# Kernel optimization log

Hardware: AMD Instinct MI355X
Metric: run time of the kernel (lower is better)

Reference implementation:

```python
import jax, jax.numpy as jnp
import numpy as np

B, H, W, C = 4, 64, 64, 128
NH, K = 4, 7
HD = C // NH
MLPD = 4 * C
EPS = 1e-5

def _ln(x, g, b):
    m = x.mean(-1, keepdims=True)
    v = ((x - m) ** 2).mean(-1, keepdims=True)
    return (x - m) * jax.lax.rsqrt(v + EPS) * g + b

def setup_inputs() -> dict:
    key = jax.random.key(0)
    ks = jax.random.split(key, 10)
    rn = lambda k, s: jax.random.normal(k, s, dtype=jnp.float32) * 0.02
    return {
        'query': jax.random.normal(ks[0], (B, H, W, C), dtype=jnp.float32),
        'key_value': jax.random.normal(ks[1], (B, H, W, C), dtype=jnp.float32),
        'g1': jnp.ones((C,), jnp.float32), 'b1': jnp.zeros((C,), jnp.float32),
        'g2': jnp.ones((C,), jnp.float32), 'b2': jnp.zeros((C,), jnp.float32),
        'g3': jnp.ones((C,), jnp.float32), 'b3': jnp.zeros((C,), jnp.float32),
        'Wq': rn(ks[2], (C, C)), 'bq': jnp.zeros((C,), jnp.float32),
        'Wkv': rn(ks[3], (C, 2 * C)), 'bkv': jnp.zeros((2 * C,), jnp.float32),
        'Wp': rn(ks[4], (C, C)), 'bp': jnp.zeros((C,), jnp.float32),
        'rpb': rn(ks[5], (NH, 2 * K - 1, 2 * K - 1)),
        'W1': rn(ks[6], (C, MLPD)), 'bm1': jnp.zeros((MLPD,), jnp.float32),
        'W2': rn(ks[7], (MLPD, C)), 'bm2': jnp.zeros((C,), jnp.float32),
    }

def _nat(qn, kvn, Wq, bq, Wkv, bkv, Wp, bp, rpb):
    # NATTEN-style 2D neighborhood attention (clamped KxK window at borders)
    q = (qn @ Wq + bq).reshape(B, H, W, NH, HD) * (HD ** -0.5)
    kv = (kvn @ Wkv + bkv).reshape(B, H, W, 2, NH, HD)
    k, v = kv[..., 0, :, :], kv[..., 1, :, :]
    ii = jnp.clip(jnp.arange(H) - K // 2, 0, H - K)[:, None] + jnp.arange(K)  # [H,K]
    jj = jnp.clip(jnp.arange(W) - K // 2, 0, W - K)[:, None] + jnp.arange(K)  # [W,K]
    def gather(t):  # [B,H,W,NH,HD] -> [B,H,W,NH,K*K,HD]
        t = jnp.take(t, ii, axis=1)   # [B,H,K,W,NH,HD]
        t = jnp.take(t, jj, axis=3)   # [B,H,K,W,K,NH,HD]
        return t.transpose(0, 1, 3, 5, 2, 4, 6).reshape(B, H, W, NH, K * K, HD)
    kn, vn = gather(k), gather(v)
    scores = jnp.einsum('bijhd,bijhnd->bijhn', q, kn)  # [B,H,W,NH,K*K]
    # relative positional bias: offsets in [-(K-1), K-1] -> index into 2K-1 table
    ri = ii - jnp.arange(H)[:, None] + (K - 1)  # [H,K]
    rj = jj - jnp.arange(W)[:, None] + (K - 1)  # [W,K]
    bias = rpb[:, ri]                   # [NH,H,K,2K-1]
    bias = jnp.take(bias, rj, axis=3)   # [NH,H,K,W,K]
    bias = bias.transpose(1, 3, 0, 2, 4).reshape(H, W, NH, K * K)
    attn = jax.nn.softmax(scores + bias[None], axis=-1)
    out = jnp.einsum('bijhn,bijhnd->bijhd', attn, vn).reshape(B, H, W, C)
    return out @ Wp + bp

def reference(query, key_value, g1, b1, g2, b2, g3, b3, Wq, bq, Wkv, bkv, Wp, bp, rpb, W1, bm1, W2, bm2):
    shortcut = key_value
    qn = _ln(query, g1, b1)
    kvn = _ln(key_value, g2, b2)
    x = shortcut + _nat(qn, kvn, Wq, bq, Wkv, bkv, Wp, bp, rpb)
    h = _ln(x, g3, b3)
    h = jax.nn.gelu(h @ W1 + bm1, approximate=False) @ W2 + bm2
    return x + h
```

## Files before the change

### kernel.cpp

```cpp
#include <hip/hip_runtime.h>
#include <math.h>

#define TOK 16384

typedef __attribute__((ext_vector_type(8))) __bf16 bf16x8;
typedef __attribute__((ext_vector_type(4))) float f32x4;

__device__ inline unsigned short f2bf(float f) {
    union { float f; unsigned int u; } v; v.f = f;
    unsigned int r = v.u + 0x7fffu + ((v.u >> 16) & 1u);
    return (unsigned short)(r >> 16);
}
__device__ inline float gelu_exact(float v) {
    return 0.5f * v * (1.0f + erff(v * 0.70710678118654752f));
}

__device__ inline void ln_body(const float* __restrict__ x, const float* __restrict__ g,
                               const float* __restrict__ b, unsigned short* __restrict__ y,
                               int tok, int lane)
{
    float2 v = ((const float2*)(x + (size_t)tok * 128))[lane];
    float s = v.x + v.y;
#pragma unroll
    for (int m = 32; m >= 1; m >>= 1) s += __shfl_xor(s, m);
    float mean = s * (1.0f / 128.0f);
    float dx = v.x - mean, dy = v.y - mean;
    float vs = dx * dx + dy * dy;
#pragma unroll
    for (int m = 32; m >= 1; m >>= 1) vs += __shfl_xor(vs, m);
    float rs = rsqrtf(vs * (1.0f / 128.0f) + 1e-5f);
    float2 gg = ((const float2*)g)[lane];
    float2 bb = ((const float2*)b)[lane];
    float ox = dx * rs * gg.x + bb.x;
    float oy = dy * rs * gg.y + bb.y;
    unsigned int pk = (unsigned int)f2bf(ox) | ((unsigned int)f2bf(oy) << 16);
    ((unsigned int*)(y + (size_t)tok * 128))[lane] = pk;
}

__global__ __launch_bounds__(256) void prep_kernel(
    const float* __restrict__ query, const float* __restrict__ key_value,
    const float* __restrict__ g1, const float* __restrict__ b1,
    const float* __restrict__ g2, const float* __restrict__ b2,
    const float* __restrict__ Wq, const float* __restrict__ Wkv,
    const float* __restrict__ Wp, const float* __restrict__ W1, const float* __restrict__ W2,
    unsigned short* __restrict__ qnh, unsigned short* __restrict__ kvnh,
    unsigned short* __restrict__ Wt)
{
    int blk = blockIdx.x, tid = threadIdx.x;
    if (blk < 8192) {
        int lane = tid & 63;
        if (blk < 4096) ln_body(query,     g1, b1, qnh,  blk * 4 + (tid >> 6), lane);
        else            ln_body(key_value, g2, b2, kvnh, (blk - 4096) * 4 + (tid >> 6), lane);
        return;
    }
    __shared__ float tile[32][33];
    int t = blk - 8192;
    const float* src; unsigned short* dst; int Kd, Nd, li;
    if      (t < 16)  { src = Wq;  dst = Wt;          Kd = 128; Nd = 128; li = t; }
    else if (t < 48)  { src = Wkv; dst = Wt + 16384;  Kd = 128; Nd = 256; li = t - 16; }
    else if (t < 64)  { src = Wp;  dst = Wt + 49152;  Kd = 128; Nd = 128; li = t - 48; }
    else if (t < 128) { src = W1;  dst = Wt + 65536;  Kd = 128; Nd = 512; li = t - 64; }
    else              { src = W2;  dst = Wt + 131072; Kd = 512; Nd = 128; li = t - 128; }
    int ntc = Nd >> 5;
    int k0 = (li / ntc) * 32, n0 = (li % ntc) * 32;
    int r = tid >> 3, c4 = (tid & 7) * 4;
    float4 v = *(const float4*)(src + (size_t)(k0 + r) * Nd + n0 + c4);
    tile[r][c4 + 0] = v.x; tile[r][c4 + 1] = v.y;
    tile[r][c4 + 2] = v.z; tile[r][c4 + 3] = v.w;
    __syncthreads();
    ushort4 o;
    o.x = f2bf(tile[c4 + 0][r]);
    o.y = f2bf(tile[c4 + 1][r]);
    o.z = f2bf(tile[c4 + 2][r]);
    o.w = f2bf(tile[c4 + 3][r]);
    *(ushort4*)(dst + (size_t)(n0 + r) * Kd + k0 + c4) = o;
}

__global__ __launch_bounds__(256) void natqkv(
    const unsigned short* __restrict__ qnh,
    const unsigned short* __restrict__ kvnh,
    const unsigned short* __restrict__ Wt,
    const float* __restrict__ bq, const float* __restrict__ bkv,
    const float* __restrict__ rpb,
    unsigned short* __restrict__ out,
    float qscale)
{
    __shared__ __align__(16) unsigned short shm[22272];
    __shared__ float rpbs[169];
    unsigned short* kS = shm;
    unsigned short* qS = shm + 8960;
    unsigned short* P  = shm;
    unsigned short* vT = shm + 14848;
    const int tid = threadIdx.x;
    const int wave = tid >> 6, lane = tid & 63;
    const int lr = lane & 15, lg = lane >> 4;
    const int bid = blockIdx.x;
    const int tile = bid & 63, h = (bid >> 6) & 3, b = bid >> 8;
    const int ti0 = (tile >> 3) * 8, tj0 = (tile & 7) * 8;
    const int hr0 = min(max(ti0 - 3, 0), 50);
    const int hc0 = min(max(tj0 - 3, 0), 50);
    const int bb = b << 12;
    if (tid < 169) rpbs[tid] = rpb[h * 169 + tid];

    const unsigned short* WtKV = Wt + 16384;

    {
        const bool vjob = wave >= 2;
        const int n0 = vjob ? 128 + h * 32 + (wave - 2) * 16 : h * 32 + wave * 16;
        const unsigned short* wrow = WtKV + (size_t)(n0 + lr) * 128;
        bf16x8 wf[4];
#pragma unroll
        for (int kk = 0; kk < 4; ++kk) wf[kk] = *(const bf16x8*)(wrow + kk * 32 + lg * 8);
#pragma unroll
        for (int rt = 0; rt < 14; ++rt) {
            int tok = bb + (hr0 + rt) * 64 + hc0 + lr;
            const unsigned short* asrc = kvnh + (size_t)tok * 128;
            f32x4 acc = {0.f, 0.f, 0.f, 0.f};
#pragma unroll
            for (int kk = 0; kk < 4; ++kk) {
                bf16x8 xf = *(const bf16x8*)(asrc + kk * 32 + lg * 8);
                acc = vjob ? __builtin_amdgcn_mfma_f32_16x16x32_bf16(xf, wf[kk], acc, 0, 0, 0)
                           : __builtin_amdgcn_mfma_f32_16x16x32_bf16(wf[kk], xf, acc, 0, 0, 0);
            }
            if (!vjob) {
                int chb = wave * 16 + lg * 4;
                float4 bs = *(const float4*)(bkv + h * 32 + chb);
                ushort4 pk;
                pk.x = f2bf(acc[0] + bs.x); pk.y = f2bf(acc[1] + bs.y);
                pk.z = f2bf(acc[2] + bs.z); pk.w = f2bf(acc[3] + bs.w);
                *(ushort4*)&kS[(rt * 16 + lr) * 40 + chb] = pk;
            } else {
                int chl = (wave - 2) * 16 + lr;
                float bs = bkv[128 + h * 32 + chl];
                ushort4 pk;
                pk.x = f2bf(acc[0] + bs); pk.y = f2bf(acc[1] + bs);
                pk.z = f2bf(acc[2] + bs); pk.w = f2bf(acc[3] + bs);
                *(ushort4*)&vT[chl * 232 + rt * 16 + lg * 4] = pk;
            }
        }
    }
    {
        const int colt = wave & 1;
        const unsigned short* wrow = Wt + (size_t)(h * 32 + colt * 16 + lr) * 128;
        bf16x8 wf[4];
#pragma unroll
        for (int kk = 0; kk < 4; ++kk) wf[kk] = *(const bf16x8*)(wrow + kk * 32 + lg * 8);
#pragma unroll
        for (int tt = 0; tt < 2; ++tt) {
            int qrt = (wave >> 1) + tt * 2;
            int qi = qrt * 16 + lr;
            int tok = bb + (ti0 + (qi >> 3)) * 64 + tj0 + (qi & 7);
            const unsigned short* asrc = qnh + (size_t)tok * 128;
            f32x4 acc = {0.f, 0.f, 0.f, 0.f};
#pragma unroll
            for (int kk = 0; kk < 4; ++kk) {
                bf16x8 xf = *(const bf16x8*)(asrc + kk * 32 + lg * 8);
                acc = __builtin_amdgcn_mfma_f32_16x16x32_bf16(wf[kk], xf, acc, 0, 0, 0);
            }
            int chb = colt * 16 + lg * 4;
            float4 bs = *(const float4*)(bq + h * 32 + chb);
            ushort4 pk;
            pk.x = f2bf((acc[0] + bs.x) * qscale); pk.y = f2bf((acc[1] + bs.y) * qscale);
            pk.z = f2bf((acc[2] + bs.z) * qscale); pk.w = f2bf((acc[3] + bs.w) * qscale);
            *(ushort4*)&qS[(qrt * 16 + lr) * 40 + chb] = pk;
        }
    }
    __syncthreads();

    bf16x8 qf = *(const bf16x8*)&qS[(wave * 16 + lr) * 40 + lg * 8];
    f32x4 S[14];
#pragma unroll
    for (int kb = 0; kb < 14; ++kb) {
        bf16x8 kf = *(const bf16x8*)&kS[(kb * 16 + lr) * 40 + lg * 8];
        f32x4 z = {0.f, 0.f, 0.f, 0.f};
        S[kb] = __builtin_amdgcn_mfma_f32_16x16x32_bf16(qf, kf, z, 0, 0, 0);
    }
    __syncthreads();

#pragma unroll
    for (int i = 0; i < 4; ++i) {
        int m = lg * 4 + i;
        int gi = ti0 + wave * 2 + (m >> 3);
        int gj = tj0 + (m & 7);
        int si = min(max(gi - 3, 0), 57), sj = min(max(gj - 3, 0), 57);
        bool cv = (unsigned)(hc0 + lr - sj) < 7u;
        int rjc = min(max(hc0 + lr - gj + 6, 0), 12);
        float mxi = -INFINITY;
#pragma unroll
        for (int kb = 0; kb < 14; ++kb) {
            bool rv = (unsigned)(hr0 + kb - si) < 7u;
            int ric = min(max(hr0 + kb - gi + 6, 0), 12);
            float bias = rpbs[rjc + ric * 13];
            float s = (rv && cv) ? S[kb][i] + bias : -1e30f;
            S[kb][i] = s;
            mxi = fmaxf(mxi, s);
        }
        mxi = fmaxf(mxi, __shfl_xor(mxi, 1));
        mxi = fmaxf(mxi, __shfl_xor(mxi, 2));
        mxi = fmaxf(mxi, __shfl_xor(mxi, 4));
        mxi = fmaxf(mxi, __shfl_xor(mxi, 8));
        float smi = 0.0f;
#pragma unroll
        for (int kb = 0; kb < 14; ++kb) {
            float e = expf(S[kb][i] - mxi);
            S[kb][i] = e;
            smi += e;
        }
        smi += __shfl_xor(smi, 1);
        smi += __shfl_xor(smi, 2);
        smi += __shfl_xor(smi, 4);
        smi += __shfl_xor(smi, 8);
        float rinv = 1.0f / smi;
#pragma unroll
        for (int kb = 0; kb < 14; ++kb)
            P[(wave * 16 + m) * 232 + kb * 16 + lr] = f2bf(S[kb][i] * rinv);
    }

    f32x4 O[2] = {};
#pragma unroll
    for (int ks = 0; ks < 7; ++ks) {
        bf16x8 pf = *(const bf16x8*)&P[(wave * 16 + lr) * 232 + ks * 32 + lg * 8];
#pragma unroll
        for (int nb = 0; nb < 2; ++nb) {
            bf16x8 vf = *(const bf16x8*)&vT[(nb * 16 + lr) * 232 + ks * 32 + lg * 8];
            O[nb] = __builtin_amdgcn_mfma_f32_16x16x32_bf16(pf, vf, O[nb], 0, 0, 0);
        }
    }
#pragma unroll
    for (int i = 0; i < 4; ++i) {
        int m = lg * 4 + i;
        int gi = ti0 + wave * 2 + (m >> 3);
        int gj = tj0 + (m & 7);
        size_t t = ((size_t)(bb + gi * 64 + gj)) * 128 + h * 32;
        out[t + lr]      = f2bf(O[0][i]);
        out[t + 16 + lr] = f2bf(O[1][i]);
    }
}

__global__ __launch_bounds__(256) void tail_kernel(
    const unsigned short* __restrict__ attnh,
    const unsigned short* __restrict__ WtP,
    const unsigned short* __restrict__ W1t,
    const unsigned short* __restrict__ W2t,
    const float* __restrict__ bp, const float* __restrict__ bm1, const float* __restrict__ bm2,
    const float* __restrict__ resk,
    const float* __restrict__ g3, const float* __restrict__ b3,
    float* __restrict__ dout)
{
    __shared__ float xs[32][132];
    __shared__ __align__(16) unsigned short xnS[32 * 136];
    __shared__ __align__(16) unsigned short hS[32 * 520];
    const int tid = threadIdx.x;
    const int wave = tid >> 6, lane = tid & 63;
    const int lr = lane & 15, lg = lane >> 4;
    const int m0 = blockIdx.x * 32;

#pragma unroll
    for (int t = 0; t < 4; ++t) {
        int j = t * 4 + wave;
        int rowt = j >> 3, colt = j & 7;
        int tok = m0 + rowt * 16 + lr;
        f32x4 acc = {0.f, 0.f, 0.f, 0.f};
#pragma unroll
        for (int kk = 0; kk < 4; ++kk) {
            bf16x8 af = *(const bf16x8*)(attnh + (size_t)tok * 128 + kk * 32 + lg * 8);
            bf16x8 wf = *(const bf16x8*)(WtP + (size_t)(colt * 16 + lr) * 128 + kk * 32 + lg * 8);
            acc = __builtin_amdgcn_mfma_f32_16x16x32_bf16(af, wf, acc, 0, 0, 0);
        }
        int gc = colt * 16 + lr;
        float bs = bp[gc];
#pragma unroll
        for (int r = 0; r < 4; ++r) {
            int row = rowt * 16 + lg * 4 + r;
            xs[row][gc] = acc[r] + bs + resk[(size_t)(m0 + row) * 128 + gc];
        }
    }
    __syncthreads();

    {
        const int r = tid >> 3, t8 = tid & 7;
        float vals[16];
#pragma unroll
        for (int jj = 0; jj < 16; ++jj) vals[jj] = xs[r][t8 * 16 + jj];
        float s = 0.0f;
#pragma unroll
        for (int jj = 0; jj < 16; ++jj) s += vals[jj];
        s += __shfl_xor(s, 1); s += __shfl_xor(s, 2); s += __shfl_xor(s, 4);
        float mean = s * (1.0f / 128.0f);
        float vv = 0.0f;
#pragma unroll
        for (int jj = 0; jj < 16; ++jj) { float d = vals[jj] - mean; vv += d * d; }
        vv += __shfl_xor(vv, 1); vv += __shfl_xor(vv, 2); vv += __shfl_xor(vv, 4);
        float rs = rsqrtf(vv * (1.0f / 128.0f) + 1e-5f);
#pragma unroll
        for (int jj = 0; jj < 4; ++jj) {
            float4 gg = ((const float4*)g3)[t8 * 4 + jj];
            float4 bb = ((const float4*)b3)[t8 * 4 + jj];
            ushort4 o;
            o.x = f2bf((vals[jj * 4 + 0] - mean) * rs * gg.x + bb.x);
            o.y = f2bf((vals[jj * 4 + 1] - mean) * rs * gg.y + bb.y);
            o.z = f2bf((vals[jj * 4 + 2] - mean) * rs * gg.z + bb.z);
            o.w = f2bf((vals[jj * 4 + 3] - mean) * rs * gg.w + bb.w);
            *(ushort4*)&xnS[r * 136 + t8 * 16 + jj * 4] = o;
        }
    }
    __syncthreads();

#pragma unroll
    for (int t = 0; t < 16; ++t) {
        int j = t * 4 + wave;
        int rowt = j >> 5, colt = j & 31;
        f32x4 acc = {0.f, 0.f, 0.f, 0.f};
#pragma unroll
        for (int kk = 0; kk < 4; ++kk) {
            bf16x8 wf = *(const bf16x8*)(W1t + (size_t)(colt * 16 + lr) * 128 + kk * 32 + lg * 8);
            bf16x8 xf = *(const bf16x8*)&xnS[(rowt * 16 + lr) * 136 + kk * 32 + lg * 8];
            acc = __builtin_amdgcn_mfma_f32_16x16x32_bf16(wf, xf, acc, 0, 0, 0);
        }
        int chb = colt * 16 + lg * 4;
        float4 bs = *(const float4*)(bm1 + chb);
        ushort4 pk;
        pk.x = f2bf(gelu_exact(acc[0] + bs.x));
        pk.y = f2bf(gelu_exact(acc[1] + bs.y));
        pk.z = f2bf(gelu_exact(acc[2] + bs.z));
        pk.w = f2bf(gelu_exact(acc[3] + bs.w));
        *(ushort4*)&hS[(rowt * 16 + lr) * 520 + chb] = pk;
    }
    __syncthreads();

#pragma unroll
    for (int t = 0; t < 4; ++t) {
        int j = t * 4 + wave;
        int rowt = j >> 3, colt = j & 7;
        f32x4 acc = {0.f, 0.f, 0.f, 0.f};
#pragma unroll
        for (int kk = 0; kk < 16; ++kk) {
            bf16x8 hf = *(const bf16x8*)&hS[(rowt * 16 + lr) * 520 + kk * 32 + lg * 8];
            bf16x8 wf = *(const bf16x8*)(W2t + (size_t)(colt * 16 + lr) * 512 + kk * 32 + lg * 8);
            acc = __builtin_amdgcn_mfma_f32_16x16x32_bf16(hf, wf, acc, 0, 0, 0);
        }
        int gc = colt * 16 + lr;
        float bs = bm2[gc];
#pragma unroll
        for (int r = 0; r < 4; ++r) {
            int row = rowt * 16 + lg * 4 + r;
            dout[(size_t)(m0 + row) * 128 + gc] = acc[r] + bs + xs[row][gc];
        }
    }
}

extern "C" void kernel_launch(void* const* d_in, const int* in_sizes, int n_in,
                              void* d_out, int out_size, void* d_ws, size_t ws_size,
                              hipStream_t stream) {
    const float* query     = (const float*)d_in[0];
    const float* key_value = (const float*)d_in[1];
    const float* g1 = (const float*)d_in[2];
    const float* b1 = (const float*)d_in[3];
    const float* g2 = (const float*)d_in[4];
    const float* b2 = (const float*)d_in[5];
    const float* g3 = (const float*)d_in[6];
    const float* b3 = (const float*)d_in[7];
    const float* Wq  = (const float*)d_in[8];
    const float* bq  = (const float*)d_in[9];
    const float* Wkv = (const float*)d_in[10];
    const float* bkv = (const float*)d_in[11];
    const float* Wp  = (const float*)d_in[12];
    const float* bp  = (const float*)d_in[13];
    const float* rpb = (const float*)d_in[14];
    const float* W1  = (const float*)d_in[15];
    const float* bm1 = (const float*)d_in[16];
    const float* W2  = (const float*)d_in[17];
    const float* bm2 = (const float*)d_in[18];

    char* ws = (char*)d_ws;
    unsigned short* qnh   = (unsigned short*)(ws + 0);
    unsigned short* kvnh  = (unsigned short*)(ws + 4194304);
    unsigned short* attnh = (unsigned short*)(ws + 8388608);
    unsigned short* Wt    = (unsigned short*)(ws + 12582912);

    const float qscale = 0.17677669529663687f;

    prep_kernel<<<8384, 256, 0, stream>>>(query, key_value, g1, b1, g2, b2,
                                          Wq, Wkv, Wp, W1, W2, qnh, kvnh, Wt);
    natqkv<<<1024, 256, 0, stream>>>(qnh, kvnh, Wt, bq, bkv, rpb, attnh, qscale);
    tail_kernel<<<512, 256, 0, stream>>>(attnh, Wt + 49152, Wt + 65536, Wt + 131072,
                                         bp, bm1, bm2, key_value, g3, b3, (float*)d_out);
}
```

Before: 198.8 us.

## Split QKV projection from attention, fuse LayerNorm into projection kernel

Moves the LayerNorm of query and key_value into a new per-token kernel that also does the Q/K/V projections. This removes the redundant halo K/V recomputation the attention kernel did for every 8x8 tile. The attention kernel now only gathers precomputed bf16 K/V, uses a smaller shared buffer with a launch-bounds occupancy hint, writes P in chunks, and uses fast exp. The tail kernel is retiled to 16 tokens per block so it launches twice as many blocks. The cost is an extra kernel launch and a global round trip for Q/K/V.

```diff
diff --git a/kernel.cpp b/kernel.cpp
--- a/kernel.cpp
+++ b/kernel.cpp
@@ -15,46 +15,13 @@
     return 0.5f * v * (1.0f + erff(v * 0.70710678118654752f));
 }
 
-__device__ inline void ln_body(const float* __restrict__ x, const float* __restrict__ g,
-                               const float* __restrict__ b, unsigned short* __restrict__ y,
-                               int tok, int lane)
-{
-    float2 v = ((const float2*)(x + (size_t)tok * 128))[lane];
-    float s = v.x + v.y;
-#pragma unroll
-    for (int m = 32; m >= 1; m >>= 1) s += __shfl_xor(s, m);
-    float mean = s * (1.0f / 128.0f);
-    float dx = v.x - mean, dy = v.y - mean;
-    float vs = dx * dx + dy * dy;
-#pragma unroll
-    for (int m = 32; m >= 1; m >>= 1) vs += __shfl_xor(vs, m);
-    float rs = rsqrtf(vs * (1.0f / 128.0f) + 1e-5f);
-    float2 gg = ((const float2*)g)[lane];
-    float2 bb = ((const float2*)b)[lane];
-    float ox = dx * rs * gg.x + bb.x;
-    float oy = dy * rs * gg.y + bb.y;
-    unsigned int pk = (unsigned int)f2bf(ox) | ((unsigned int)f2bf(oy) << 16);
-    ((unsigned int*)(y + (size_t)tok * 128))[lane] = pk;
-}
-
-__global__ __launch_bounds__(256) void prep_kernel(
-    const float* __restrict__ query, const float* __restrict__ key_value,
-    const float* __restrict__ g1, const float* __restrict__ b1,
-    const float* __restrict__ g2, const float* __restrict__ b2,
+__global__ __launch_bounds__(256) void wtrans_kernel(
     const float* __restrict__ Wq, const float* __restrict__ Wkv,
     const float* __restrict__ Wp, const float* __restrict__ W1, const float* __restrict__ W2,
-    unsigned short* __restrict__ qnh, unsigned short* __restrict__ kvnh,
     unsigned short* __restrict__ Wt)
 {
-    int blk = blockIdx.x, tid = threadIdx.x;
-    if (blk < 8192) {
-        int lane = tid & 63;
-        if (blk < 4096) ln_body(query,     g1, b1, qnh,  blk * 4 + (tid >> 6), lane);
-        else            ln_body(key_value, g2, b2, kvnh, (blk - 4096) * 4 + (tid >> 6), lane);
-        return;
-    }
     __shared__ float tile[32][33];
-    int t = blk - 8192;
+    int t = blockIdx.x, tid = threadIdx.x;
     const float* src; unsigned short* dst; int Kd, Nd, li;
     if      (t < 16)  { src = Wq;  dst = Wt;          Kd = 128; Nd = 128; li = t; }
     else if (t < 48)  { src = Wkv; dst = Wt + 16384;  Kd = 128; Nd = 256; li = t - 16; }
@@ -76,21 +43,104 @@
     *(ushort4*)(dst + (size_t)(n0 + r) * Kd + k0 + c4) = o;
 }
 
-__global__ __launch_bounds__(256) void natqkv(
-    const unsigned short* __restrict__ qnh,
-    const unsigned short* __restrict__ kvnh,
+__global__ __launch_bounds__(256) void qkvln_kernel(
+    const float* __restrict__ query, const float* __restrict__ key_value,
+    const float* __restrict__ g1, const float* __restrict__ b1,
+    const float* __restrict__ g2, const float* __restrict__ b2,
     const unsigned short* __restrict__ Wt,
     const float* __restrict__ bq, const float* __restrict__ bkv,
+    unsigned short* __restrict__ qbh, unsigned short* __restrict__ kbh,
+    unsigned short* __restrict__ vbh, float qscale)
+{
+    __shared__ __align__(16) unsigned short aq[16 * 136];
+    __shared__ __align__(16) unsigned short akv[16 * 136];
+    const int tid = threadIdx.x;
+    const int wave = tid >> 6, lane = tid & 63;
+    const int lr = lane & 15, lg = lane >> 4;
+    const int m0 = blockIdx.x * 16;
+
+    {
+        const int r = tid >> 4, t16 = tid & 15;
+#pragma unroll
+        for (int which = 0; which < 2; ++which) {
+            const float* xr = (which ? key_value : query) + (size_t)(m0 + r) * 128 + t16 * 8;
+            float4 v0 = *(const float4*)xr;
+            float4 v1 = *(const float4*)(xr + 4);
+            float s = v0.x + v0.y + v0.z + v0.w + v1.x + v1.y + v1.z + v1.w;
+            s += __shfl_xor(s, 1); s += __shfl_xor(s, 2);
+            s += __shfl_xor(s, 4); s += __shfl_xor(s, 8);
+            float mean = s * (1.0f / 128.0f);
+            float d0 = v0.x - mean, d1 = v0.y - mean, d2 = v0.z - mean, d3 = v0.w - mean;
+            float d4 = v1.x - mean, d5 = v1.y - mean, d6 = v1.z - mean, d7 = v1.w - mean;
+            float vv = d0*d0 + d1*d1 + d2*d2 + d3*d3 + d4*d4 + d5*d5 + d6*d6 + d7*d7;
+            vv += __shfl_xor(vv, 1); vv += __shfl_xor(vv, 2);
+            vv += __shfl_xor(vv, 4); vv += __shfl_xor(vv, 8);
+            float rs = rsqrtf(vv * (1.0f / 128.0f) + 1e-5f);
+            const float* g = which ? g2 : g1;
+            const float* bb = which ? b2 : b1;
+            float4 ga = *(const float4*)(g + t16 * 8);
+            float4 gb = *(const float4*)(g + t16 * 8 + 4);
+            float4 ba = *(const float4*)(bb + t16 * 8);
+            float4 bbb = *(const float4*)(bb + t16 * 8 + 4);
+            ushort4 oa, ob;
+            oa.x = f2bf(d0 * rs * ga.x + ba.x); oa.y = f2bf(d1 * rs * ga.y + ba.y);
+            oa.z = f2bf(d2 * rs * ga.z + ba.z); oa.w = f2bf(d3 * rs * ga.w + ba.w);
+            ob.x = f2bf(d4 * rs * gb.x + bbb.x); ob.y = f2bf(d5 * rs * gb.y + bbb.y);
+            ob.z = f2bf(d6 * rs * gb.z + bbb.z); ob.w = f2bf(d7 * rs * gb.w + bbb.w);
+            unsigned short* dst = (which ? akv : aq) + r * 136 + t16 * 8;
+            *(ushort4*)dst = oa;
+            *(ushort4*)(dst + 4) = ob;
+        }
+    }
+    __syncthreads();
+
+#pragma unroll
+    for (int t = 0; t < 6; ++t) {
+        int j = wave + 4 * t;
+        const unsigned short* A = (j < 8) ? aq : akv;
+        const unsigned short* Wb = (j < 8) ? (Wt + (size_t)(j * 16 + lr) * 128)
+                                           : (Wt + 16384 + (size_t)((j - 8) * 16 + lr) * 128);
+        f32x4 acc = {0.f, 0.f, 0.f, 0.f};
+#pragma unroll
+        for (int kk = 0; kk < 4; ++kk) {
+            bf16x8 af = *(const bf16x8*)&A[lr * 136 + kk * 32 + lg * 8];
+            bf16x8 wf = *(const bf16x8*)(Wb + kk * 32 + lg * 8);
+            acc = __builtin_amdgcn_mfma_f32_16x16x32_bf16(af, wf, acc, 0, 0, 0);
+        }
+        if (j < 8) {
+            int gc = j * 16 + lr;
+            float bs = bq[gc];
+#pragma unroll
+            for (int r = 0; r < 4; ++r)
+                qbh[(size_t)(m0 + lg * 4 + r) * 128 + gc] = f2bf((acc[r] + bs) * qscale);
+        } else {
+            int gc = (j - 8) * 16 + lr;
+            float bs = bkv[gc];
+            if (gc < 128) {
+#pragma unroll
+                for (int r = 0; r < 4; ++r)
+                    kbh[(size_t)(m0 + lg * 4 + r) * 128 + gc] = f2bf(acc[r] + bs);
+            } else {
+#pragma unroll
+                for (int r = 0; r < 4; ++r)
+                    vbh[(size_t)(m0 + lg * 4 + r) * 128 + gc - 128] = f2bf(acc[r] + bs);
+            }
+        }
+    }
+}
+
+__global__ __launch_bounds__(256, 4) void nat_attn(
+    const unsigned short* __restrict__ qbh,
+    const unsigned short* __restrict__ kbh,
+    const unsigned short* __restrict__ vbh,
     const float* __restrict__ rpb,
-    unsigned short* __restrict__ out,
-    float qscale)
+    unsigned short* __restrict__ out)
 {
-    __shared__ __align__(16) unsigned short shm[22272];
-    __shared__ float rpbs[169];
+    __shared__ __align__(16) unsigned short shm[16384];
     unsigned short* kS = shm;
-    unsigned short* qS = shm + 8960;
-    unsigned short* P  = shm;
-    unsigned short* vT = shm + 14848;
+    unsigned short* vT = shm + 8960;
+    unsigned short* Pb = shm;
+    float* rpbs = (float*)(shm + 4608);
     const int tid = threadIdx.x;
     const int wave = tid >> 6, lane = tid & 63;
     const int lr = lane & 15, lg = lane >> 4;
@@ -100,74 +150,26 @@
     const int hr0 = min(max(ti0 - 3, 0), 50);
     const int hc0 = min(max(tj0 - 3, 0), 50);
     const int bb = b << 12;
-    if (tid < 169) rpbs[tid] = rpb[h * 169 + tid];
-
-    const unsigned short* WtKV = Wt + 16384;
-
-    {
-        const bool vjob = wave >= 2;
-        const int n0 = vjob ? 128 + h * 32 + (wave - 2) * 16 : h * 32 + wave * 16;
-        const unsigned short* wrow = WtKV + (size_t)(n0 + lr) * 128;
-        bf16x8 wf[4];
-#pragma unroll
-        for (int kk = 0; kk < 4; ++kk) wf[kk] = *(const bf16x8*)(wrow + kk * 32 + lg * 8);
-#pragma unroll
-        for (int rt = 0; rt < 14; ++rt) {
-            int tok = bb + (hr0 + rt) * 64 + hc0 + lr;
-            const unsigned short* asrc = kvnh + (size_t)tok * 128;
-            f32x4 acc = {0.f, 0.f, 0.f, 0.f};
-#pragma unroll
-            for (int kk = 0; kk < 4; ++kk) {
-                bf16x8 xf = *(const bf16x8*)(asrc + kk * 32 + lg * 8);
-                acc = vjob ? __builtin_amdgcn_mfma_f32_16x16x32_bf16(xf, wf[kk], acc, 0, 0, 0)
-                           : __builtin_amdgcn_mfma_f32_16x16x32_bf16(wf[kk], xf, acc, 0, 0, 0);
-            }
-            if (!vjob) {
-                int chb = wave * 16 + lg * 4;
-                float4 bs = *(const float4*)(bkv + h * 32 + chb);
-                ushort4 pk;
-                pk.x = f2bf(acc[0] + bs.x); pk.y = f2bf(acc[1] + bs.y);
-                pk.z = f2bf(acc[2] + bs.z); pk.w = f2bf(acc[3] + bs.w);
-                *(ushort4*)&kS[(rt * 16 + lr) * 40 + chb] = pk;
-            } else {
-                int chl = (wave - 2) * 16 + lr;
-                float bs = bkv[128 + h * 32 + chl];
-                ushort4 pk;
-                pk.x = f2bf(acc[0] + bs); pk.y = f2bf(acc[1] + bs);
-                pk.z = f2bf(acc[2] + bs); pk.w = f2bf(acc[3] + bs);
-                *(ushort4*)&vT[chl * 232 + rt * 16 + lg * 4] = pk;
-            }
-        }
-    }
-    {
-        const int colt = wave & 1;
-        const unsigned short* wrow = Wt + (size_t)(h * 32 + colt * 16 + lr) * 128;
-        bf16x8 wf[4];
-#pragma unroll
-        for (int kk = 0; kk < 4; ++kk) wf[kk] = *(const bf16x8*)(wrow + kk * 32 + lg * 8);
-#pragma unroll
-        for (int tt = 0; tt < 2; ++tt) {
-            int qrt = (wave >> 1) + tt * 2;
-            int qi = qrt * 16 + lr;
-            int tok = bb + (ti0 + (qi >> 3)) * 64 + tj0 + (qi & 7);
-            const unsigned short* asrc = qnh + (size_t)tok * 128;
-            f32x4 acc = {0.f, 0.f, 0.f, 0.f};
-#pragma unroll
-            for (int kk = 0; kk < 4; ++kk) {
-                bf16x8 xf = *(const bf16x8*)(asrc + kk * 32 + lg * 8);
-                acc = __builtin_amdgcn_mfma_f32_16x16x32_bf16(wf[kk], xf, acc, 0, 0, 0);
-            }
-            int chb = colt * 16 + lg * 4;
-            float4 bs = *(const float4*)(bq + h * 32 + chb);
-            ushort4 pk;
-            pk.x = f2bf((acc[0] + bs.x) * qscale); pk.y = f2bf((acc[1] + bs.y) * qscale);
-            pk.z = f2bf((acc[2] + bs.z) * qscale); pk.w = f2bf((acc[3] + bs.w) * qscale);
-            *(ushort4*)&qS[(qrt * 16 + lr) * 40 + chb] = pk;
-        }
-    }
-    __syncthreads();
-
-    bf16x8 qf = *(const bf16x8*)&qS[(wave * 16 + lr) * 40 + lg * 8];
+
+    for (int u = tid; u < 896; u += 256) {
+        int tok = u >> 2, chunk = u & 3;
+        int tr = tok >> 4, tc = tok & 15;
+        size_t src = (size_t)(bb + (hr0 + tr) * 64 + hc0 + tc) * 128 + h * 32 + chunk * 8;
+        int4 kw = *(const int4*)(kbh + src);
+        *(int4*)&kS[tok * 40 + chunk * 8] = kw;
+        int4 vw = *(const int4*)(vbh + src);
+        const unsigned short* v8 = (const unsigned short*)&vw;
+#pragma unroll
+        for (int k = 0; k < 8; ++k)
+            vT[(chunk * 8 + k) * 232 + tok] = v8[k];
+    }
+
+    const int gi_m = ti0 + wave * 2 + (lr >> 3);
+    const int gj_m = tj0 + (lr & 7);
+    const int tq = bb + gi_m * 64 + gj_m;
+    bf16x8 qf = *(const bf16x8*)(qbh + (size_t)tq * 128 + h * 32 + lg * 8);
+    __syncthreads();
+
     f32x4 S[14];
 #pragma unroll
     for (int kb = 0; kb < 14; ++kb) {
@@ -175,6 +177,9 @@
         f32x4 z = {0.f, 0.f, 0.f, 0.f};
         S[kb] = __builtin_amdgcn_mfma_f32_16x16x32_bf16(qf, kf, z, 0, 0, 0);
     }
+    __syncthreads();
+
+    if (tid < 169) rpbs[tid] = rpb[h * 169 + tid];
     __syncthreads();
 
 #pragma unroll
@@ -202,7 +207,7 @@
         float smi = 0.0f;
 #pragma unroll
         for (int kb = 0; kb < 14; ++kb) {
-            float e = expf(S[kb][i] - mxi);
+            float e = __expf(S[kb][i] - mxi);
             S[kb][i] = e;
             smi += e;
         }
@@ -212,20 +217,35 @@
         smi += __shfl_xor(smi, 8);
         float rinv = 1.0f / smi;
 #pragma unroll
-        for (int kb = 0; kb < 14; ++kb)
-            P[(wave * 16 + m) * 232 + kb * 16 + lr] = f2bf(S[kb][i] * rinv);
+        for (int kb = 0; kb < 14; ++kb) S[kb][i] *= rinv;
     }
 
     f32x4 O[2] = {};
 #pragma unroll
-    for (int ks = 0; ks < 7; ++ks) {
-        bf16x8 pf = *(const bf16x8*)&P[(wave * 16 + lr) * 232 + ks * 32 + lg * 8];
-#pragma unroll
-        for (int nb = 0; nb < 2; ++nb) {
-            bf16x8 vf = *(const bf16x8*)&vT[(nb * 16 + lr) * 232 + ks * 32 + lg * 8];
-            O[nb] = __builtin_amdgcn_mfma_f32_16x16x32_bf16(pf, vf, O[nb], 0, 0, 0);
-        }
-    }
+    for (int r = 0; r < 4; ++r) {
+        const int nk = (r < 3) ? 4 : 2;
+#pragma unroll
+        for (int i = 0; i < 4; ++i) {
+            int m = lg * 4 + i;
+#pragma unroll
+            for (int kbl = 0; kbl < 4; ++kbl) {
+                if (kbl < nk)
+                    Pb[(wave * 16 + m) * 72 + kbl * 16 + lr] = f2bf(S[r * 4 + kbl][i]);
+            }
+        }
+#pragma unroll
+        for (int ksl = 0; ksl < 2; ++ksl) {
+            if (ksl * 2 < nk) {
+                bf16x8 pf = *(const bf16x8*)&Pb[(wave * 16 + lr) * 72 + ksl * 32 + lg * 8];
+#pragma unroll
+                for (int nb = 0; nb < 2; ++nb) {
+                    bf16x8 vf = *(const bf16x8*)&vT[(nb * 16 + lr) * 232 + r * 64 + ksl * 32 + lg * 8];
+                    O[nb] = __builtin_amdgcn_mfma_f32_16x16x32_bf16(pf, vf, O[nb], 0, 0, 0);
+                }
+            }
+        }
+    }
+
 #pragma unroll
     for (int i = 0; i < 4; ++i) {
         int m = lg * 4 + i;
@@ -247,19 +267,18 @@
     const float* __restrict__ g3, const float* __restrict__ b3,
     float* __restrict__ dout)
 {
-    __shared__ float xs[32][132];
-    __shared__ __align__(16) unsigned short xnS[32 * 136];
-    __shared__ __align__(16) unsigned short hS[32 * 520];
+    __shared__ float xs[16][132];
+    __shared__ __align__(16) unsigned short xnS[16 * 136];
+    __shared__ __align__(16) unsigned short hS[16 * 520];
     const int tid = threadIdx.x;
     const int wave = tid >> 6, lane = tid & 63;
     const int lr = lane & 15, lg = lane >> 4;
-    const int m0 = blockIdx.x * 32;
-
-#pragma unroll
-    for (int t = 0; t < 4; ++t) {
-        int j = t * 4 + wave;
-        int rowt = j >> 3, colt = j & 7;
-        int tok = m0 + rowt * 16 + lr;
+    const int m0 = blockIdx.x * 16;
+
+#pragma unroll
+    for (int t = 0; t < 2; ++t) {
+        int colt = wave + 4 * t;
+        int tok = m0 + lr;
         f32x4 acc = {0.f, 0.f, 0.f, 0.f};
 #pragma unroll
         for (int kk = 0; kk < 4; ++kk) {
@@ -271,50 +290,55 @@
         float bs = bp[gc];
 #pragma unroll
         for (int r = 0; r < 4; ++r) {
-            int row = rowt * 16 + lg * 4 + r;
+            int row = lg * 4 + r;
             xs[row][gc] = acc[r] + bs + resk[(size_t)(m0 + row) * 128 + gc];
         }
     }
     __syncthreads();
 
     {
-        const int r = tid >> 3, t8 = tid & 7;
-        float vals[16];
-#pragma unroll
-        for (int jj = 0; jj < 16; ++jj) vals[jj] = xs[r][t8 * 16 + jj];
+        const int r = tid >> 4, t16 = tid & 15;
+        float vals[8];
+#pragma unroll
+        for (int jj = 0; jj < 8; ++jj) vals[jj] = xs[r][t16 * 8 + jj];
         float s = 0.0f;
 #pragma unroll
-        for (int jj = 0; jj < 16; ++jj) s += vals[jj];
-        s += __shfl_xor(s, 1); s += __shfl_xor(s, 2); s += __shfl_xor(s, 4);
+        for (int jj = 0; jj < 8; ++jj) s += vals[jj];
+        s += __shfl_xor(s, 1); s += __shfl_xor(s, 2);
+        s += __shfl_xor(s, 4); s += __shfl_xor(s, 8);
         float mean = s * (1.0f / 128.0f);
         float vv = 0.0f;
 #pragma unroll
-        for (int jj = 0; jj < 16; ++jj) { float d = vals[jj] - mean; vv += d * d; }
-        vv += __shfl_xor(vv, 1); vv += __shfl_xor(vv, 2); vv += __shfl_xor(vv, 4);
+        for (int jj = 0; jj < 8; ++jj) { float d = vals[jj] - mean; vv += d * d; }
+        vv += __shfl_xor(vv, 1); vv += __shfl_xor(vv, 2);
+        vv += __shfl_xor(vv, 4); vv += __shfl_xor(vv, 8);
         float rs = rsqrtf(vv * (1.0f / 128.0f) + 1e-5f);
-#pragma unroll
-        for (int jj = 0; jj < 4; ++jj) {
-            float4 gg = ((const float4*)g3)[t8 * 4 + jj];
-            float4 bb = ((const float4*)b3)[t8 * 4 + jj];
-            ushort4 o;
-            o.x = f2bf((vals[jj * 4 + 0] - mean) * rs * gg.x + bb.x);
-            o.y = f2bf((vals[jj * 4 + 1] - mean) * rs * gg.y + bb.y);
-            o.z = f2bf((vals[jj * 4 + 2] - mean) * rs * gg.z + bb.z);
-            o.w = f2bf((vals[jj * 4 + 3] - mean) * rs * gg.w + bb.w);
-            *(ushort4*)&xnS[r * 136 + t8 * 16 + jj * 4] = o;
-        }
-    }
-    __syncthreads();
-
-#pragma unroll
-    for (int t = 0; t < 16; ++t) {
-        int j = t * 4 + wave;
-        int rowt = j >> 5, colt = j & 31;
+        float4 ga = *(const float4*)(g3 + t16 * 8);
+        float4 gb = *(const float4*)(g3 + t16 * 8 + 4);
+        float4 ba = *(const float4*)(b3 + t16 * 8);
+        float4 bbv = *(const float4*)(b3 + t16 * 8 + 4);
+        ushort4 oa, ob;
+        oa.x = f2bf((vals[0] - mean) * rs * ga.x + ba.x);
+        oa.y = f2bf((vals[1] - mean) * rs * ga.y + ba.y);
+        oa.z = f2bf((vals[2] - mean) * rs * ga.z + ba.z);
+        oa.w = f2bf((vals[3] - mean) * rs * ga.w + ba.w);
+        ob.x = f2bf((vals[4] - mean) * rs * gb.x + bbv.x);
+        ob.y = f2bf((vals[5] - mean) * rs * gb.y + bbv.y);
+        ob.z = f2bf((vals[6] - mean) * rs * gb.z + bbv.z);
+        ob.w = f2bf((vals[7] - mean) * rs * gb.w + bbv.w);
+        *(ushort4*)&xnS[r * 136 + t16 * 8] = oa;
+        *(ushort4*)&xnS[r * 136 + t16 * 8 + 4] = ob;
+    }
+    __syncthreads();
+
+#pragma unroll
+    for (int t = 0; t < 8; ++t) {
+        int colt = wave + 4 * t;
         f32x4 acc = {0.f, 0.f, 0.f, 0.f};
 #pragma unroll
         for (int kk = 0; kk < 4; ++kk) {
             bf16x8 wf = *(const bf16x8*)(W1t + (size_t)(colt * 16 + lr) * 128 + kk * 32 + lg * 8);
-            bf16x8 xf = *(const bf16x8*)&xnS[(rowt * 16 + lr) * 136 + kk * 32 + lg * 8];
+            bf16x8 xf = *(const bf16x8*)&xnS[lr * 136 + kk * 32 + lg * 8];
             acc = __builtin_amdgcn_mfma_f32_16x16x32_bf16(wf, xf, acc, 0, 0, 0);
         }
         int chb = colt * 16 + lg * 4;
@@ -324,18 +348,17 @@
         pk.y = f2bf(gelu_exact(acc[1] + bs.y));
         pk.z = f2bf(gelu_exact(acc[2] + bs.z));
         pk.w = f2bf(gelu_exact(acc[3] + bs.w));
-        *(ushort4*)&hS[(rowt * 16 + lr) * 520 + chb] = pk;
-    }
-    __syncthreads();
-
-#pragma unroll
-    for (int t = 0; t < 4; ++t) {
-        int j = t * 4 + wave;
-        int rowt = j >> 3, colt = j & 7;
+        *(ushort4*)&hS[lr * 520 + chb] = pk;
+    }
+    __syncthreads();
+
+#pragma unroll
+    for (int t = 0; t < 2; ++t) {
+        int colt = wave + 4 * t;
         f32x4 acc = {0.f, 0.f, 0.f, 0.f};
 #pragma unroll
         for (int kk = 0; kk < 16; ++kk) {
-            bf16x8 hf = *(const bf16x8*)&hS[(rowt * 16 + lr) * 520 + kk * 32 + lg * 8];
+            bf16x8 hf = *(const bf16x8*)&hS[lr * 520 + kk * 32 + lg * 8];
             bf16x8 wf = *(const bf16x8*)(W2t + (size_t)(colt * 16 + lr) * 512 + kk * 32 + lg * 8);
             acc = __builtin_amdgcn_mfma_f32_16x16x32_bf16(hf, wf, acc, 0, 0, 0);
         }
@@ -343,7 +366,7 @@
         float bs = bm2[gc];
 #pragma unroll
         for (int r = 0; r < 4; ++r) {
-            int row = rowt * 16 + lg * 4 + r;
+            int row = lg * 4 + r;
             dout[(size_t)(m0 + row) * 128 + gc] = acc[r] + bs + xs[row][gc];
         }
     }
@@ -373,16 +396,18 @@
     const float* bm2 = (const float*)d_in[18];
 
     char* ws = (char*)d_ws;
-    unsigned short* qnh   = (unsigned short*)(ws + 0);
-    unsigned short* kvnh  = (unsigned short*)(ws + 4194304);
-    unsigned short* attnh = (unsigned short*)(ws + 8388608);
-    unsigned short* Wt    = (unsigned short*)(ws + 12582912);
+    unsigned short* qbh   = (unsigned short*)(ws + 0);
+    unsigned short* kbh   = (unsigned short*)(ws + 4194304);
+    unsigned short* vbh   = (unsigned short*)(ws + 8388608);
+    unsigned short* attnh = (unsigned short*)(ws + 12582912);
+    unsigned short* Wt    = (unsigned short*)(ws + 16777216);
 
     const float qscale = 0.17677669529663687f;
 
-    prep_kernel<<<8384, 256, 0, stream>>>(query, key_value, g1, b1, g2, b2,
-                                          Wq, Wkv, Wp, W1, W2, qnh, kvnh, Wt);
-    natqkv<<<1024, 256, 0, stream>>>(qnh, kvnh, Wt, bq, bkv, rpb, attnh, qscale);
-    tail_kernel<<<512, 256, 0, stream>>>(attnh, Wt + 49152, Wt + 65536, Wt + 131072,
-                                         bp, bm1, bm2, key_value, g3, b3, (float*)d_out);
-}
+    wtrans_kernel<<<192, 256, 0, stream>>>(Wq, Wkv, Wp, W1, W2, Wt);
+    qkvln_kernel<<<1024, 256, 0, stream>>>(query, key_value, g1, b1, g2, b2,
+                                           Wt, bq, bkv, qbh, kbh, vbh, qscale);
+    nat_attn<<<1024, 256, 0, stream>>>(qbh, kbh, vbh, rpb, attnh);
+    tail_kernel<<<1024, 256, 0, stream>>>(attnh, Wt + 49152, Wt + 65536, Wt + 131072,
+                                          bp, bm1, bm2, key_value, g3, b3, (float*)d_out);
+}
```

Measured after the change: 167.8 us. -15.6%, faster.
